# Kernel tuning notes

Hardware: AMD Instinct MI355X
Metric: run time of the kernel (lower is better)

## Reference

```python
import jax, jax.numpy as jnp
import numpy as np

B = 64          # batch
IN_CH = 128     # in_channels
OUT_CH = 128    # out_channels
MODES = 64      # modes1
N = 4096        # spatial length (power of two -> pad branches in original are no-ops)


def _fht1d(x):
    """Faithful vectorized version of the recursive fht1d.

    x: (M, n) with n a power of two. Same DIT recursion as the torch code:
    X = [E + cas*O, E - cas*O], cas(theta) = cos(theta) + sin(theta).
    Even/odd halves are stacked along the leading axis so the recursion is
    traced only log2(n) times (fully vectorized at each level).
    """
    n = x.shape[-1]
    if n == 1:
        return x
    sub = _fht1d(jnp.concatenate([x[:, 0::2], x[:, 1::2]], axis=0))  # (2M, n/2)
    e, o = jnp.split(sub, 2, axis=0)
    k = jnp.arange(n // 2, dtype=x.dtype)
    theta = (2.0 * jnp.pi / n) * k
    cas = jnp.cos(theta) + jnp.sin(theta)
    t = cas * o
    return jnp.concatenate([e + t, e - t], axis=-1)


def dht_last(x):
    """DHT along the last dim of x (B, C, N); N is a power of two."""
    shp = x.shape
    return _fht1d(x.reshape(-1, shp[-1])).reshape(shp)


def compl_mul1d(x1, x2):
    # x1: (b, i, m), x2: (i, o, m); Hartley-domain "complex" multiply.
    neg = lambda a: jnp.roll(jnp.flip(a, axis=-1), 1, axis=-1)  # H(-k)
    x1n = neg(x1)
    x2n = neg(x2)
    return 0.5 * (
        jnp.einsum('bix,iox->box', x1, x2)
        - jnp.einsum('bix,iox->box', x1n, x2n)
        + jnp.einsum('bix,iox->box', x1, x2n)
        + jnp.einsum('bix,iox->box', x1n, x2)
    )


def setup_inputs() -> dict:
    key = jax.random.key(0)
    kx, kw = jax.random.split(key)
    x = jax.random.normal(kx, (B, IN_CH, N), dtype=jnp.float32)
    scale = 1.0 / (IN_CH * OUT_CH)
    weights1 = scale * jax.random.uniform(kw, (IN_CH, OUT_CH, MODES), dtype=jnp.float32)
    return {"x": x, "weights1": weights1}


def reference(x, weights1):
    n = x.shape[-1]
    modes = weights1.shape[-1]
    x_ht = dht_last(x)                                  # (B, IN_CH, N)
    mixed = compl_mul1d(x_ht[:, :, :modes], weights1)   # (B, OUT_CH, modes)
    out_ht = jnp.zeros((x.shape[0], weights1.shape[1], n), dtype=x.dtype)
    out_ht = out_ht.at[:, :, :modes].set(mixed)
    # idht = dht / N
    return dht_last(out_ht) / n
```

## Files before the change

### kernel.cpp

```cpp
#include <hip/hip_runtime.h>
#include <math.h>

#define PI2F 6.28318530717958647692f

__host__ __device__ constexpr int br6(int p) {
    return ((p & 1) << 5) | ((p & 2) << 3) | ((p & 4) << 1) |
           ((p & 8) >> 1) | ((p & 16) >> 3) | ((p & 32) >> 5);
}
__host__ __device__ constexpr int brN(int v, int bits) {
    int r = 0;
    for (int i = 0; i < bits; ++i) r |= ((v >> i) & 1) << (bits - 1 - i);
    return r;
}

__device__ static constexpr float CAS8T[4] = {1.f, 1.41421356f, 1.f, 0.f};
__device__ static constexpr float CAS16T[8] = {
    1.f, 1.30656296f, 1.41421356f, 1.30656296f, 1.f, 0.54119610f, 0.f, -0.54119610f};
__device__ static constexpr float CAS32T[16] = {
    1.f, 1.17587560f, 1.30656296f, 1.38703985f, 1.41421356f, 1.38703985f,
    1.30656296f, 1.17587560f, 1.f, 0.78569496f, 0.54119610f, 0.27589938f,
    0.f, -0.27589938f, -0.54119610f, -0.78569496f};
__device__ static constexpr float CAS64T[32] = {
    1.f, 1.09320187f, 1.17587560f, 1.24722502f, 1.30656296f, 1.35331800f,
    1.38703985f, 1.40740373f, 1.41421356f, 1.40740373f, 1.38703985f,
    1.35331800f, 1.30656296f, 1.24722502f, 1.17587560f, 1.09320187f,
    1.f, 0.89716759f, 0.78569496f, 0.66665566f, 0.54119610f, 0.41052452f,
    0.27589938f, 0.13861717f, 0.f, -0.13861717f, -0.27589938f, -0.41052452f,
    -0.54119610f, -0.66665566f, -0.78569496f, -0.89716759f};

__global__ void casgen(float* __restrict__ casA, float* __restrict__ casT) {
    const int r = threadIdx.x;
    const int g = blockIdx.x;
    float s, c;
    if (g < 6) {
        sincosf(PI2F * (float)r / (float)(4096 >> g), &s, &c);
        casA[g * 64 + r] = c + s;
    } else {
        const int j = g - 6;
        int l, u;
        if (j == 0) { l = 5; u = 0; }
        else if (j < 3) { l = 4; u = j - 1; }
        else if (j < 7) { l = 3; u = j - 3; }
        else if (j < 15) { l = 2; u = j - 7; }
        else if (j < 31) { l = 1; u = j - 15; }
        else { l = 0; u = j - 31; }
        sincosf(PI2F * (float)(r + 64 * u) / (float)(4096 >> l), &s, &c);
        casT[j * 64 + r] = c + s;
    }
}

__global__ void wtrans(const float* __restrict__ w,
                       float* __restrict__ wp, float* __restrict__ wm) {
    const int i = blockIdx.x;
    const int m = blockIdx.y;
    const int o = threadIdx.x;
    const int mp = (64 - m) & 63;
    const float a = w[(i * 128 + o) * 64 + m];
    const float b = w[(i * 128 + o) * 64 + mp];
    wp[((size_t)m * 128 + i) * 128 + o] = 0.5f * (a + b);
    wm[((size_t)m * 128 + i) * 128 + o] = 0.5f * (a - b);
}

__global__ __launch_bounds__(64) void fht_fwd(const float* __restrict__ x,
                                              const float* __restrict__ casA,
                                              float* __restrict__ xh_t) {
    __shared__ float Y[64 * 65];
    const int lane = threadIdx.x;

    float a6[6];
#pragma unroll
    for (int l = 0; l < 6; ++l) a6[l] = casA[l * 64 + lane];
    float G[64];
    G[0] = 1.0f;
#pragma unroll
    for (int c = 1; c < 64; ++c) G[c] = G[c & (c - 1)] * a6[__builtin_ctz(c)];

    const int row0 = blockIdx.x * 2;
#pragma unroll 1
    for (int rr = 0; rr < 2; ++rr) {
        const int row = row0 + rr;
        const float* xr = x + (size_t)row * 4096 + lane;
        float v[64];
#pragma unroll
        for (int p = 0; p < 64; ++p) v[p] = xr[64 * br6(p)];

#pragma unroll
        for (int b = 0; b < 64; b += 2) {
            float t0 = v[b], t1 = v[b + 1];
            v[b] = t0 + t1; v[b + 1] = t0 - t1;
        }
#pragma unroll
        for (int b = 0; b < 64; b += 4)
#pragma unroll
            for (int k = 0; k < 2; ++k) {
                float t0 = v[b + k], t1 = v[b + k + 2];
                v[b + k] = t0 + t1; v[b + k + 2] = t0 - t1;
            }
#pragma unroll
        for (int b = 0; b < 64; b += 8)
#pragma unroll
            for (int k = 0; k < 4; ++k) {
                float w = CAS8T[k];
                float t0 = v[b + k], t1 = v[b + k + 4];
                v[b + k] = fmaf(w, t1, t0); v[b + k + 4] = fmaf(-w, t1, t0);
            }
#pragma unroll
        for (int b = 0; b < 64; b += 16)
#pragma unroll
            for (int k = 0; k < 8; ++k) {
                float w = CAS16T[k];
                float t0 = v[b + k], t1 = v[b + k + 8];
                v[b + k] = fmaf(w, t1, t0); v[b + k + 8] = fmaf(-w, t1, t0);
            }
#pragma unroll
        for (int b = 0; b < 64; b += 32)
#pragma unroll
            for (int k = 0; k < 16; ++k) {
                float w = CAS32T[k];
                float t0 = v[b + k], t1 = v[b + k + 16];
                v[b + k] = fmaf(w, t1, t0); v[b + k + 16] = fmaf(-w, t1, t0);
            }
#pragma unroll
        for (int k = 0; k < 32; ++k) {
            float w = CAS64T[k];
            float t0 = v[k], t1 = v[k + 32];
            v[k] = fmaf(w, t1, t0); v[k + 32] = fmaf(-w, t1, t0);
        }

#pragma unroll
        for (int m = 0; m < 64; ++m) Y[lane * 65 + m] = v[m];
        __syncthreads();
        float acc = 0.0f;
#pragma unroll
        for (int c = 0; c < 64; ++c) acc = fmaf(G[c], Y[c * 65 + lane], acc);
        __syncthreads();
        xh_t[(size_t)lane * 8192 + row] = acc;
    }
}

__global__ __launch_bounds__(256) void passB(const float* __restrict__ xh_t,
                                             const float* __restrict__ wp,
                                             const float* __restrict__ wm,
                                             float* __restrict__ mixed_t) {
    __shared__ float Us[64][33];
    __shared__ float Uns[64][33];
    const int tid = threadIdx.x;
    const int m = blockIdx.y;
    const int iBase = blockIdx.x * 32;
    const int mp = (64 - m) & 63;
#pragma unroll
    for (int it = 0; it < 2; ++it) {
        const int slot = tid + it * 256;
        const int b = slot >> 3;
        const int i4 = slot & 7;
        const float4 vu = *(const float4*)(xh_t + (size_t)m * 8192 + b * 128 + iBase + 4 * i4);
        const float4 vn = *(const float4*)(xh_t + (size_t)mp * 8192 + b * 128 + iBase + 4 * i4);
        Us[b][i4 * 4 + 0] = vu.x; Us[b][i4 * 4 + 1] = vu.y;
        Us[b][i4 * 4 + 2] = vu.z; Us[b][i4 * 4 + 3] = vu.w;
        Uns[b][i4 * 4 + 0] = vn.x; Uns[b][i4 * 4 + 1] = vn.y;
        Uns[b][i4 * 4 + 2] = vn.z; Uns[b][i4 * 4 + 3] = vn.w;
    }
    __syncthreads();
    const int o0 = (tid & 15) * 8;
    const int b0 = (tid >> 4) * 4;
    float acc[4][8];
#pragma unroll
    for (int a = 0; a < 4; ++a)
#pragma unroll
        for (int b = 0; b < 8; ++b) acc[a][b] = 0.0f;

    for (int i = 0; i < 32; ++i) {
        const int ig = iBase + i;
        float p[8], q[8];
        *(float4*)&p[0] = *(const float4*)(wp + ((size_t)m * 128 + ig) * 128 + o0);
        *(float4*)&p[4] = *(const float4*)(wp + ((size_t)m * 128 + ig) * 128 + o0 + 4);
        *(float4*)&q[0] = *(const float4*)(wm + ((size_t)m * 128 + ig) * 128 + o0);
        *(float4*)&q[4] = *(const float4*)(wm + ((size_t)m * 128 + ig) * 128 + o0 + 4);
#pragma unroll
        for (int jb = 0; jb < 4; ++jb) {
            const float u = Us[b0 + jb][i];
            const float un = Uns[b0 + jb][i];
#pragma unroll
            for (int jo = 0; jo < 8; ++jo)
                acc[jb][jo] += u * p[jo] + un * q[jo];
        }
    }
#pragma unroll
    for (int jb = 0; jb < 4; ++jb)
#pragma unroll
        for (int jo = 0; jo < 8; ++jo)
            atomicAdd(&mixed_t[(size_t)m * 8192 + (b0 + jb) * 128 + o0 + jo], acc[jb][jo]);
}

__global__ __launch_bounds__(64) void fht_inv(const float* __restrict__ mixed_t,
                                              const float* __restrict__ casT,
                                              float* __restrict__ out) {
    __shared__ __align__(16) float S[64];
    const int lane = threadIdx.x;
    float K[63];
#pragma unroll
    for (int j = 0; j < 63; ++j) K[j] = casT[j * 64 + lane];

    const int row0 = blockIdx.x * 4;
#pragma unroll 1
    for (int rr = 0; rr < 4; ++rr) {
        const int row = row0 + rr;
        const float mv = mixed_t[(size_t)lane * 8192 + row] * (1.0f / 4096.0f);
        __syncthreads();
        S[lane] = mv;
        __syncthreads();
        float e[64];
#pragma unroll
        for (int m4 = 0; m4 < 16; ++m4) {
            const float4 q = *(const float4*)&S[4 * m4];
            e[4 * m4 + 0] = q.x; e[4 * m4 + 1] = q.y;
            e[4 * m4 + 2] = q.z; e[4 * m4 + 3] = q.w;
        }
#pragma unroll
        for (int mp = 0; mp < 32; ++mp) {
            float w = K[0];
            float t0 = e[mp], t1 = e[mp + 32];
            e[mp] = fmaf(w, t1, t0); e[mp + 32] = fmaf(-w, t1, t0);
        }
#pragma unroll
        for (int hi = 0; hi < 2; ++hi)
#pragma unroll
            for (int mp = 0; mp < 16; ++mp) {
                float w = K[1 + brN(hi, 1)];
                int i0 = hi * 32 + mp;
                float t0 = e[i0], t1 = e[i0 + 16];
                e[i0] = fmaf(w, t1, t0); e[i0 + 16] = fmaf(-w, t1, t0);
            }
#pragma unroll
        for (int hi = 0; hi < 4; ++hi)
#pragma unroll
            for (int mp = 0; mp < 8; ++mp) {
                float w = K[3 + brN(hi, 2)];
                int i0 = hi * 16 + mp;
                float t0 = e[i0], t1 = e[i0 + 8];
                e[i0] = fmaf(w, t1, t0); e[i0 + 8] = fmaf(-w, t1, t0);
            }
#pragma unroll
        for (int hi = 0; hi < 8; ++hi)
#pragma unroll
            for (int mp = 0; mp < 4; ++mp) {
                float w = K[7 + brN(hi, 3)];
                int i0 = hi * 8 + mp;
                float t0 = e[i0], t1 = e[i0 + 4];
                e[i0] = fmaf(w, t1, t0); e[i0 + 4] = fmaf(-w, t1, t0);
            }
#pragma unroll
        for (int hi = 0; hi < 16; ++hi)
#pragma unroll
            for (int mp = 0; mp < 2; ++mp) {
                float w = K[15 + brN(hi, 4)];
                int i0 = hi * 4 + mp;
                float t0 = e[i0], t1 = e[i0 + 2];
                e[i0] = fmaf(w, t1, t0); e[i0 + 2] = fmaf(-w, t1, t0);
            }
#pragma unroll
        for (int hi = 0; hi < 32; ++hi) {
            float w = K[31 + brN(hi, 5)];
            int i0 = hi * 2;
            float t0 = e[i0], t1 = e[i0 + 1];
            e[i0] = fmaf(w, t1, t0); e[i0 + 1] = fmaf(-w, t1, t0);
        }
        float* outr = out + (size_t)row * 4096 + lane;
#pragma unroll
        for (int t = 0; t < 64; ++t) outr[64 * t] = e[br6(t)];
    }
}

extern "C" void kernel_launch(void* const* d_in, const int* in_sizes, int n_in,
                              void* d_out, int out_size, void* d_ws, size_t ws_size,
                              hipStream_t stream) {
    const float* x = (const float*)d_in[0];
    const float* w = (const float*)d_in[1];
    float* out = (float*)d_out;
    float* wsf = (float*)d_ws;

    float* casA    = wsf;
    float* casT    = wsf + 512;
    float* xh_t    = wsf + 8192;
    float* wp      = wsf + 532480;
    float* wm      = wsf + 1581056;
    float* mixed_t = wsf + 2629632;

    hipMemsetAsync(mixed_t, 0, 524288 * sizeof(float), stream);

    casgen<<<dim3(69), dim3(64), 0, stream>>>(casA, casT);
    wtrans<<<dim3(128, 64), dim3(128), 0, stream>>>(w, wp, wm);
    fht_fwd<<<dim3(4096), dim3(64), 0, stream>>>(x, casA, xh_t);
    passB<<<dim3(4, 64), dim3(256), 0, stream>>>(xh_t, wp, wm, mixed_t);
    fht_inv<<<dim3(2048), dim3(64), 0, stream>>>(mixed_t, casT, out);
}
```

Before: 327.1 us.

## Drop memset and casgen launch, coalesce weight transpose, remove atomics in mixing

Merges the cas-table generation into the weight-transpose kernel and computes the forward twiddles inline with sincosf, which removes one kernel launch and the memset. The weight transpose now stages a tile in shared memory so the global reads are coalesced float4 loads. The mixing kernel switches from splitting the input-channel reduction across blocks with atomicAdd to having each block own 16 batch rows over the full 128 channels, writing results with plain float4 stores. The trade-off is that each block now streams the full weight slice for its mode, increasing per-block weight reads, and each thread holds fewer accumulators.

```diff
diff --git a/kernel.cpp b/kernel.cpp
--- a/kernel.cpp
+++ b/kernel.cpp
@@ -28,48 +28,74 @@
     0.27589938f, 0.13861717f, 0.f, -0.13861717f, -0.27589938f, -0.41052452f,
     -0.54119610f, -0.66665566f, -0.78569496f, -0.89716759f};
 
-__global__ void casgen(float* __restrict__ casA, float* __restrict__ casT) {
-    const int r = threadIdx.x;
-    const int g = blockIdx.x;
-    float s, c;
-    if (g < 6) {
-        sincosf(PI2F * (float)r / (float)(4096 >> g), &s, &c);
-        casA[g * 64 + r] = c + s;
-    } else {
-        const int j = g - 6;
-        int l, u;
-        if (j == 0) { l = 5; u = 0; }
-        else if (j < 3) { l = 4; u = j - 1; }
-        else if (j < 7) { l = 3; u = j - 3; }
-        else if (j < 15) { l = 2; u = j - 7; }
-        else if (j < 31) { l = 1; u = j - 15; }
-        else { l = 0; u = j - 31; }
-        sincosf(PI2F * (float)(r + 64 * u) / (float)(4096 >> l), &s, &c);
-        casT[j * 64 + r] = c + s;
-    }
-}
-
-__global__ void wtrans(const float* __restrict__ w,
-                       float* __restrict__ wp, float* __restrict__ wm) {
+__global__ __launch_bounds__(256) void wtrans_cast(const float* __restrict__ w,
+                                                   float* __restrict__ wp,
+                                                   float* __restrict__ wm,
+                                                   float* __restrict__ casT) {
+    const int tid = threadIdx.x;
+    if (blockIdx.x == 128) {
+        if (blockIdx.y != 0) return;
+#pragma unroll
+        for (int base = 0; base < 4096; base += 256) {
+            const int idx = base + tid;
+            if (idx < 4032) {
+                const int j = idx >> 6, r = idx & 63;
+                int l, u;
+                if (j == 0) { l = 5; u = 0; }
+                else if (j < 3) { l = 4; u = j - 1; }
+                else if (j < 7) { l = 3; u = j - 3; }
+                else if (j < 15) { l = 2; u = j - 7; }
+                else if (j < 31) { l = 1; u = j - 15; }
+                else { l = 0; u = j - 31; }
+                float s, c;
+                sincosf(PI2F * (float)(r + 64 * u) / (float)(4096 >> l), &s, &c);
+                casT[j * 64 + r] = c + s;
+            }
+        }
+        return;
+    }
+    __shared__ float W[64 * 65];
     const int i = blockIdx.x;
-    const int m = blockIdx.y;
-    const int o = threadIdx.x;
-    const int mp = (64 - m) & 63;
-    const float a = w[(i * 128 + o) * 64 + m];
-    const float b = w[(i * 128 + o) * 64 + mp];
-    wp[((size_t)m * 128 + i) * 128 + o] = 0.5f * (a + b);
-    wm[((size_t)m * 128 + i) * 128 + o] = 0.5f * (a - b);
+    const int oh = blockIdx.y;
+    const float* src = w + (size_t)i * 8192 + oh * 4096;
+#pragma unroll
+    for (int it = 0; it < 4; ++it) {
+        const int k = it * 1024 + tid * 4;
+        const float4 v = *(const float4*)(src + k);
+        const int ol = k >> 6;
+        const int ml = k & 63;
+        W[ol * 65 + ml + 0] = v.x;
+        W[ol * 65 + ml + 1] = v.y;
+        W[ol * 65 + ml + 2] = v.z;
+        W[ol * 65 + ml + 3] = v.w;
+    }
+    __syncthreads();
+    const int mh = tid >> 6;
+    const int ol = tid & 63;
+    const int o = oh * 64 + ol;
+#pragma unroll
+    for (int ml = 0; ml < 16; ++ml) {
+        const int m = mh * 16 + ml;
+        const int mp = (64 - m) & 63;
+        const float a = W[ol * 65 + m];
+        const float b = W[ol * 65 + mp];
+        wp[((size_t)m * 128 + i) * 128 + o] = 0.5f * (a + b);
+        wm[((size_t)m * 128 + i) * 128 + o] = 0.5f * (a - b);
+    }
 }
 
 __global__ __launch_bounds__(64) void fht_fwd(const float* __restrict__ x,
-                                              const float* __restrict__ casA,
                                               float* __restrict__ xh_t) {
     __shared__ float Y[64 * 65];
     const int lane = threadIdx.x;
 
     float a6[6];
 #pragma unroll
-    for (int l = 0; l < 6; ++l) a6[l] = casA[l * 64 + lane];
+    for (int l = 0; l < 6; ++l) {
+        float s, c;
+        sincosf(PI2F * (float)lane / (float)(4096 >> l), &s, &c);
+        a6[l] = c + s;
+    }
     float G[64];
     G[0] = 1.0f;
 #pragma unroll
@@ -142,54 +168,43 @@
                                              const float* __restrict__ wp,
                                              const float* __restrict__ wm,
                                              float* __restrict__ mixed_t) {
-    __shared__ float Us[64][33];
-    __shared__ float Uns[64][33];
+    __shared__ float Us[16][136];
+    __shared__ float Uns[16][136];
     const int tid = threadIdx.x;
     const int m = blockIdx.y;
-    const int iBase = blockIdx.x * 32;
+    const int bt = blockIdx.x;
     const int mp = (64 - m) & 63;
 #pragma unroll
     for (int it = 0; it < 2; ++it) {
         const int slot = tid + it * 256;
-        const int b = slot >> 3;
-        const int i4 = slot & 7;
-        const float4 vu = *(const float4*)(xh_t + (size_t)m * 8192 + b * 128 + iBase + 4 * i4);
-        const float4 vn = *(const float4*)(xh_t + (size_t)mp * 8192 + b * 128 + iBase + 4 * i4);
-        Us[b][i4 * 4 + 0] = vu.x; Us[b][i4 * 4 + 1] = vu.y;
-        Us[b][i4 * 4 + 2] = vu.z; Us[b][i4 * 4 + 3] = vu.w;
-        Uns[b][i4 * 4 + 0] = vn.x; Uns[b][i4 * 4 + 1] = vn.y;
-        Uns[b][i4 * 4 + 2] = vn.z; Uns[b][i4 * 4 + 3] = vn.w;
+        const int b = slot >> 5;
+        const int i0 = (slot & 31) * 4;
+        const float4 vu = *(const float4*)(xh_t + (size_t)m  * 8192 + bt * 2048 + slot * 4);
+        const float4 vn = *(const float4*)(xh_t + (size_t)mp * 8192 + bt * 2048 + slot * 4);
+        *(float4*)&Us[b][i0] = vu;
+        *(float4*)&Uns[b][i0] = vn;
     }
     __syncthreads();
+    const int b = tid >> 4;
     const int o0 = (tid & 15) * 8;
-    const int b0 = (tid >> 4) * 4;
-    float acc[4][8];
-#pragma unroll
-    for (int a = 0; a < 4; ++a)
-#pragma unroll
-        for (int b = 0; b < 8; ++b) acc[a][b] = 0.0f;
-
-    for (int i = 0; i < 32; ++i) {
-        const int ig = iBase + i;
+    float acc[8];
+#pragma unroll
+    for (int j = 0; j < 8; ++j) acc[j] = 0.0f;
+#pragma unroll 2
+    for (int i = 0; i < 128; ++i) {
         float p[8], q[8];
-        *(float4*)&p[0] = *(const float4*)(wp + ((size_t)m * 128 + ig) * 128 + o0);
-        *(float4*)&p[4] = *(const float4*)(wp + ((size_t)m * 128 + ig) * 128 + o0 + 4);
-        *(float4*)&q[0] = *(const float4*)(wm + ((size_t)m * 128 + ig) * 128 + o0);
-        *(float4*)&q[4] = *(const float4*)(wm + ((size_t)m * 128 + ig) * 128 + o0 + 4);
-#pragma unroll
-        for (int jb = 0; jb < 4; ++jb) {
-            const float u = Us[b0 + jb][i];
-            const float un = Uns[b0 + jb][i];
-#pragma unroll
-            for (int jo = 0; jo < 8; ++jo)
-                acc[jb][jo] += u * p[jo] + un * q[jo];
-        }
-    }
-#pragma unroll
-    for (int jb = 0; jb < 4; ++jb)
-#pragma unroll
-        for (int jo = 0; jo < 8; ++jo)
-            atomicAdd(&mixed_t[(size_t)m * 8192 + (b0 + jb) * 128 + o0 + jo], acc[jb][jo]);
+        *(float4*)&p[0] = *(const float4*)(wp + ((size_t)m * 128 + i) * 128 + o0);
+        *(float4*)&p[4] = *(const float4*)(wp + ((size_t)m * 128 + i) * 128 + o0 + 4);
+        *(float4*)&q[0] = *(const float4*)(wm + ((size_t)m * 128 + i) * 128 + o0);
+        *(float4*)&q[4] = *(const float4*)(wm + ((size_t)m * 128 + i) * 128 + o0 + 4);
+        const float u = Us[b][i];
+        const float un = Uns[b][i];
+#pragma unroll
+        for (int j = 0; j < 8; ++j) acc[j] += u * p[j] + un * q[j];
+    }
+    float* dst = mixed_t + (size_t)m * 8192 + (bt * 16 + b) * 128 + o0;
+    *(float4*)dst = make_float4(acc[0], acc[1], acc[2], acc[3]);
+    *(float4*)(dst + 4) = make_float4(acc[4], acc[5], acc[6], acc[7]);
 }
 
 __global__ __launch_bounds__(64) void fht_inv(const float* __restrict__ mixed_t,
@@ -279,18 +294,14 @@
     float* out = (float*)d_out;
     float* wsf = (float*)d_ws;
 
-    float* casA    = wsf;
     float* casT    = wsf + 512;
     float* xh_t    = wsf + 8192;
     float* wp      = wsf + 532480;
     float* wm      = wsf + 1581056;
     float* mixed_t = wsf + 2629632;
 
-    hipMemsetAsync(mixed_t, 0, 524288 * sizeof(float), stream);
-
-    casgen<<<dim3(69), dim3(64), 0, stream>>>(casA, casT);
-    wtrans<<<dim3(128, 64), dim3(128), 0, stream>>>(w, wp, wm);
-    fht_fwd<<<dim3(4096), dim3(64), 0, stream>>>(x, casA, xh_t);
+    wtrans_cast<<<dim3(129, 2), dim3(256), 0, stream>>>(w, wp, wm, casT);
+    fht_fwd<<<dim3(4096), dim3(64), 0, stream>>>(x, xh_t);
     passB<<<dim3(4, 64), dim3(256), 0, stream>>>(xh_t, wp, wm, mixed_t);
     fht_inv<<<dim3(2048), dim3(64), 0, stream>>>(mixed_t, casT, out);
 }
```

New measurement: 274.4 us. 1.19x faster.
